# Kernel tuning notes

Measured on AMD Instinct MI355X. Metric: run time of the kernel, lower is better.

## Reference

```python
import jax, jax.numpy as jnp
import numpy as np

P_L = P_R = P_T = P_D = 1  # lrtd_pad = 1
N_BATCH, C, H, W = 2, 64, 256, 256


def _pad_cube(x):
    """x: [6, C, H, W], face order: front, right, back, left, top, down.
    Returns [6, C, H+p_t+p_d, W+p_l+p_r]."""
    p_l, p_r, p_t, p_d = P_L, P_R, P_T, P_D
    f_front, f_right, f_back, f_left, f_top, f_down = (x[i] for i in range(6))
    T = lambda a: jnp.transpose(a, (0, 2, 1))  # swap last two dims of [C,*,*]

    # top plate: [6, C, p_t, W]
    t = jnp.stack([
        f_top[:, -p_t:, :],
        jnp.flip(T(f_top[:, :, -p_t:]), 2),
        jnp.flip(f_top[:, :p_t, :], 2),
        jnp.flip(T(f_top[:, :, :p_t]), 1),
        jnp.flip(f_back[:, :p_t, :], (1, 2)),
        f_front[:, -p_t:, :],
    ], 0)
    # down plate: [6, C, p_d, W]
    d = jnp.stack([
        f_down[:, :p_d, :],
        jnp.flip(T(f_down[:, :, -p_d:]), 1),
        jnp.flip(f_down[:, -p_d:, :], (1, 2)),
        jnp.flip(T(f_down[:, :, :p_d]), 2),
        f_front[:, :p_d, :],
        jnp.flip(f_back[:, -p_d:, :], (1, 2)),
    ], 0)
    # left plate: [6, C, H, p_l]
    l = jnp.stack([
        f_left[:, :, -p_l:],
        f_front[:, :, -p_l:],
        f_right[:, :, -p_l:],
        f_back[:, :, -p_l:],
        T(f_left[:, :p_l, :]),
        jnp.flip(T(f_left[:, -p_l:, :]), 1),
    ], 0)
    # right plate: [6, C, H, p_r]
    r = jnp.stack([
        f_right[:, :, :p_r],
        f_back[:, :, :p_r],
        f_left[:, :, :p_r],
        f_front[:, :, :p_r],
        jnp.flip(T(f_right[:, :p_r, :]), 1),
        T(jnp.flip(f_right[:, -p_r:, :], 1)),
    ], 0)

    def edge(td, lr):  # corner construction (make_cubepad_edge)
        tdp, lrp = td.shape[2], lr.shape[3]
        if tdp > lrp:
            return jnp.tile(lr, (1, 1, tdp, 1))
        return jnp.tile(td, (1, 1, 1, lrp))

    p_tr = edge(t[:, :, -p_t:, -1:], r[:, :, :1, :p_r])
    p_tl = edge(t[:, :, :p_t, :1], l[:, :, :1, :p_l])
    p_dr = edge(d[:, :, -p_d:, -1:], r[:, :, -1:, -p_r:])
    p_dl = edge(d[:, :, :p_d, :1], l[:, :, -1:, -p_l:])

    lcol = jnp.concatenate([p_tl, l, p_dl], 2)   # [6, C, H+p_t+p_d, p_l]
    rcol = jnp.concatenate([p_tr, r, p_dr], 2)   # [6, C, H+p_t+p_d, p_r]
    mid = jnp.concatenate([t, x, d], 2)          # [6, C, H+p_t+p_d, W]
    return jnp.concatenate([lcol, mid, rcol], 3)


def setup_inputs() -> dict:
    key = jax.random.key(0)
    x = jax.random.normal(key, (6 * N_BATCH, C, H, W), dtype=jnp.float32)
    return {"x": x}


def reference(x) -> jnp.ndarray:
    n = x.shape[0] // 6
    xb = x.reshape(n, 6, *x.shape[1:])
    out = jax.vmap(_pad_cube)(xb)  # [N, 6, C, H', W']
    return out.reshape(n * 6, *out.shape[2:])
```

## Files before the change

kernel.cpp:

```cpp
#include <hip/hip_runtime.h>


#define C_  64
#define H_  256
#define W_  256
#define HP  258
#define WP  258
#define FACE_STRIDE (C_ * H_ * W_)
#define PLANE_IN  (H_ * W_)
#define PLANE_OUT (HP * WP)

__global__ void cubepad_row_kernel(const float* __restrict__ x,
                                   float* __restrict__ out) {
  const int t   = threadIdx.x;
  const int h   = blockIdx.x;
  const int fgc = blockIdx.y;
  const int fg  = fgc >> 6;
  const int c   = fgc & 63;
  const int face = fg < 6 ? fg : fg - 6;
  const int nb   = fg < 6 ? 0 : 1;

  const float* base = x + (size_t)nb * 6 * FACE_STRIDE + (size_t)c * PLANE_IN;
  float* orow = out + (size_t)fgc * PLANE_OUT + (size_t)h * WP;
#define IN(f, hh, ww) base[(size_t)(f) * FACE_STRIDE + (hh) * W_ + (ww)]

  if (h > 0 && h < HP - 1) {
    const int hi = h - 1;
    orow[t + 1] = IN(face, hi, t);
    if (t == 0) {
      float v;
      switch (face) {
        case 0:  v = IN(3, hi, 255);       break;
        case 1:  v = IN(0, hi, 255);       break;
        case 2:  v = IN(1, hi, 255);       break;
        case 3:  v = IN(2, hi, 255);       break;
        case 4:  v = IN(3, 0, hi);         break;
        default: v = IN(3, 255, 255 - hi); break;
      }
      orow[0] = v;
    } else if (t == 255) {
      float v;
      switch (face) {
        case 0:  v = IN(1, hi, 0);         break;
        case 1:  v = IN(2, hi, 0);         break;
        case 2:  v = IN(3, hi, 0);         break;
        case 3:  v = IN(0, hi, 0);         break;
        case 4:  v = IN(1, 0, 255 - hi);   break;
        default: v = IN(1, 255, hi);       break;
      }
      orow[257] = v;
    }
  } else if (h == 0) {
    const int wi = t;
    float v;
    switch (face) {
      case 0:  v = IN(4, 255, wi);        break;
      case 1:  v = IN(4, 255 - wi, 255);  break;
      case 2:  v = IN(4, 0, 255 - wi);    break;
      case 3:  v = IN(4, wi, 0);          break;
      case 4:  v = IN(2, 0, 255 - wi);    break;
      default: v = IN(0, 255, wi);        break;
    }
    orow[t + 1] = v;
    if (t == 0)   orow[0]   = v;
    if (t == 255) orow[257] = v;
  } else {
    const int wi = t;
    float v;
    switch (face) {
      case 0:  v = IN(5, 0, wi);          break;
      case 1:  v = IN(5, wi, 255);        break;
      case 2:  v = IN(5, 255, 255 - wi);  break;
      case 3:  v = IN(5, 255 - wi, 0);    break;
      case 4:  v = IN(0, 0, wi);          break;
      default: v = IN(2, 255, 255 - wi);  break;
    }
    orow[t + 1] = v;
    if (t == 0)   orow[0]   = v;
    if (t == 255) orow[257] = v;
  }
#undef IN
}

extern "C" void kernel_launch(void* const* d_in, const int* in_sizes, int n_in,
                              void* d_out, int out_size, void* d_ws, size_t ws_size,
                              hipStream_t stream) {
  const float* x = (const float*)d_in[0];
  float* out = (float*)d_out;
  dim3 grid(HP, 768);
  cubepad_row_kernel<<<grid, 256, 0, stream>>>(x, out);
}
```

Before: 418.6 us.

## Flatten output plane and write float4 vectors with per-element fallback at borders

Replaces the one-block-per-output-row scheme with a flat mapping where each thread produces four consecutive output floats of a channel plane. Since the 258x258 plane is a multiple of 4 elements, stores are aligned 16-byte vector writes. Interior reads become unaligned 4-wide loads, and border elements fall back to a per-element routine. The intent is fewer memory instructions and fewer idle threads on this memory-bound copy, at the cost of div/mod index math, unaligned loads and some divergence at row edges.

```diff
diff --git a/kernel.cpp b/kernel.cpp
--- a/kernel.cpp
+++ b/kernel.cpp
@@ -9,77 +9,88 @@
 #define FACE_STRIDE (C_ * H_ * W_)
 #define PLANE_IN  (H_ * W_)
 #define PLANE_OUT (HP * WP)
+#define P4_PER_PLANE (PLANE_OUT / 4)
 
-__global__ void cubepad_row_kernel(const float* __restrict__ x,
-                                   float* __restrict__ out) {
-  const int t   = threadIdx.x;
-  const int h   = blockIdx.x;
+typedef float f4  __attribute__((ext_vector_type(4)));
+typedef float f4u __attribute__((ext_vector_type(4), aligned(4)));
+
+__device__ __forceinline__ float value_at(const float* __restrict__ base,
+                                          int face, int h, int w) {
+#define IN(f, hh, ww) base[(size_t)(f) * FACE_STRIDE + (hh) * W_ + (ww)]
+  if (h >= 1 && h <= H_ && w >= 1 && w <= W_) return IN(face, h - 1, w - 1);
+  if (h == 0) {
+    int wi = w - 1; wi = wi < 0 ? 0 : (wi > 255 ? 255 : wi);
+    switch (face) {
+      case 0:  return IN(4, 255, wi);
+      case 1:  return IN(4, 255 - wi, 255);
+      case 2:  return IN(4, 0, 255 - wi);
+      case 3:  return IN(4, wi, 0);
+      case 4:  return IN(2, 0, 255 - wi);
+      default: return IN(0, 255, wi);
+    }
+  }
+  if (h == HP - 1) {
+    int wi = w - 1; wi = wi < 0 ? 0 : (wi > 255 ? 255 : wi);
+    switch (face) {
+      case 0:  return IN(5, 0, wi);
+      case 1:  return IN(5, wi, 255);
+      case 2:  return IN(5, 255, 255 - wi);
+      case 3:  return IN(5, 255 - wi, 0);
+      case 4:  return IN(0, 0, wi);
+      default: return IN(2, 255, 255 - wi);
+    }
+  }
+  int hi = h - 1;
+  if (w == 0) {
+    switch (face) {
+      case 0:  return IN(3, hi, 255);
+      case 1:  return IN(0, hi, 255);
+      case 2:  return IN(1, hi, 255);
+      case 3:  return IN(2, hi, 255);
+      case 4:  return IN(3, 0, hi);
+      default: return IN(3, 255, 255 - hi);
+    }
+  }
+  switch (face) {
+    case 0:  return IN(1, hi, 0);
+    case 1:  return IN(2, hi, 0);
+    case 2:  return IN(3, hi, 0);
+    case 3:  return IN(0, hi, 0);
+    case 4:  return IN(1, 0, 255 - hi);
+    default: return IN(1, 255, hi);
+  }
+#undef IN
+}
+
+__global__ void cubepad_v4_kernel(const float* __restrict__ x,
+                                  float* __restrict__ out) {
+  int p4 = blockIdx.x * blockDim.x + threadIdx.x;
+  if (p4 >= P4_PER_PLANE) return;
   const int fgc = blockIdx.y;
   const int fg  = fgc >> 6;
   const int c   = fgc & 63;
   const int face = fg < 6 ? fg : fg - 6;
   const int nb   = fg < 6 ? 0 : 1;
+  const float* base = x + (size_t)nb * 6 * FACE_STRIDE + (size_t)c * PLANE_IN;
 
-  const float* base = x + (size_t)nb * 6 * FACE_STRIDE + (size_t)c * PLANE_IN;
-  float* orow = out + (size_t)fgc * PLANE_OUT + (size_t)h * WP;
-#define IN(f, hh, ww) base[(size_t)(f) * FACE_STRIDE + (hh) * W_ + (ww)]
+  const unsigned p = (unsigned)p4 << 2;
+  const unsigned h = p / WP;
+  const unsigned w = p - h * WP;
 
-  if (h > 0 && h < HP - 1) {
-    const int hi = h - 1;
-    orow[t + 1] = IN(face, hi, t);
-    if (t == 0) {
-      float v;
-      switch (face) {
-        case 0:  v = IN(3, hi, 255);       break;
-        case 1:  v = IN(0, hi, 255);       break;
-        case 2:  v = IN(1, hi, 255);       break;
-        case 3:  v = IN(2, hi, 255);       break;
-        case 4:  v = IN(3, 0, hi);         break;
-        default: v = IN(3, 255, 255 - hi); break;
-      }
-      orow[0] = v;
-    } else if (t == 255) {
-      float v;
-      switch (face) {
-        case 0:  v = IN(1, hi, 0);         break;
-        case 1:  v = IN(2, hi, 0);         break;
-        case 2:  v = IN(3, hi, 0);         break;
-        case 3:  v = IN(0, hi, 0);         break;
-        case 4:  v = IN(1, 0, 255 - hi);   break;
-        default: v = IN(1, 255, hi);       break;
-      }
-      orow[257] = v;
+  f4 v;
+  if (h >= 1u && h <= 256u && w >= 1u && w <= 253u) {
+    v = *(const f4u*)(base + (size_t)face * FACE_STRIDE +
+                      (size_t)(h - 1) * W_ + (w - 1));
+  } else {
+#pragma unroll
+    for (int e = 0; e < 4; ++e) {
+      unsigned pe = p + e;
+      unsigned he = pe / WP;
+      unsigned we = pe - he * WP;
+      v[e] = value_at(base, face, (int)he, (int)we);
     }
-  } else if (h == 0) {
-    const int wi = t;
-    float v;
-    switch (face) {
-      case 0:  v = IN(4, 255, wi);        break;
-      case 1:  v = IN(4, 255 - wi, 255);  break;
-      case 2:  v = IN(4, 0, 255 - wi);    break;
-      case 3:  v = IN(4, wi, 0);          break;
-      case 4:  v = IN(2, 0, 255 - wi);    break;
-      default: v = IN(0, 255, wi);        break;
-    }
-    orow[t + 1] = v;
-    if (t == 0)   orow[0]   = v;
-    if (t == 255) orow[257] = v;
-  } else {
-    const int wi = t;
-    float v;
-    switch (face) {
-      case 0:  v = IN(5, 0, wi);          break;
-      case 1:  v = IN(5, wi, 255);        break;
-      case 2:  v = IN(5, 255, 255 - wi);  break;
-      case 3:  v = IN(5, 255 - wi, 0);    break;
-      case 4:  v = IN(0, 0, wi);          break;
-      default: v = IN(2, 255, 255 - wi);  break;
-    }
-    orow[t + 1] = v;
-    if (t == 0)   orow[0]   = v;
-    if (t == 255) orow[257] = v;
   }
-#undef IN
+  *(f4*)(out + (size_t)fgc * PLANE_OUT + p) = v;
 }
 
 extern "C" void kernel_launch(void* const* d_in, const int* in_sizes, int n_in,
@@ -87,6 +98,6 @@
                               hipStream_t stream) {
   const float* x = (const float*)d_in[0];
   float* out = (float*)d_out;
-  dim3 grid(HP, 768);
-  cubepad_row_kernel<<<grid, 256, 0, stream>>>(x, out);
+  dim3 grid((P4_PER_PLANE + 255) / 256, 768);
+  cubepad_v4_kernel<<<grid, 256, 0, stream>>>(x, out);
 }
```

After: 339.4 us. -18.9%, faster.
